# Kernel tuning notes

Hardware: AMD Instinct MI355X
Metric: run time of the kernel (lower is better)

## Reference

```python
import jax, jax.numpy as jnp
import numpy as np

N = 20000          # nodes
E = 320000         # edges (avg degree 16)
MUL = 64           # multiplicity of 0e and 1o in hidden irreps
NUM_BASIS = 8
HID = 64           # radial MLP hidden
NSPEC = 4          # node attribute (species) scalars
N_NEIGH = 16.0
SILU_NORM = 1.679177  # e3nn normalize2mom constant for silu


def silu_n(x):
    return jax.nn.silu(x) * SILU_NORM


def setup_inputs() -> dict:
    key = jax.random.key(0)
    ks = jax.random.split(key, 20)
    inp = {
        'node_scalars': jax.random.normal(ks[0], (N, MUL), jnp.float32),
        'node_vectors': jax.random.normal(ks[1], (N, MUL, 3), jnp.float32),
        'node_attr': jax.random.uniform(ks[2], (N, NSPEC), jnp.float32),
        'edge_sh': jax.random.normal(ks[3], (E, 4), jnp.float32),
        'edge_embedded': jax.random.uniform(ks[4], (E, NUM_BASIS), jnp.float32),
        'edge_src': jax.random.randint(ks[5], (E,), 0, N),
        'edge_dst': jax.random.randint(ks[6], (E,), 0, N),
        # e3nn Linear #1 (64x0e+64x1o -> same)
        'W_lin1_s': jax.random.normal(ks[7], (MUL, MUL), jnp.float32),
        'W_lin1_v': jax.random.normal(ks[8], (MUL, MUL), jnp.float32),
        # radial FullyConnectedNet 8 -> 64 -> 64 -> 256
        'W_fc0': jax.random.normal(ks[9], (NUM_BASIS, HID), jnp.float32),
        'W_fc1': jax.random.normal(ks[10], (HID, HID), jnp.float32),
        'W_fc2': jax.random.normal(ks[11], (HID, 4 * MUL), jnp.float32),
        # e3nn Linear #2 (128x0e+128x1o -> 128x0e+64x1o)
        'W_lin2_s': jax.random.normal(ks[12], (2 * MUL, 2 * MUL), jnp.float32),
        'W_lin2_v': jax.random.normal(ks[13], (2 * MUL, MUL), jnp.float32),
        # self-connection FullyConnectedTensorProduct weights
        'W_sc_s': jax.random.normal(ks[14], (MUL, NSPEC, 2 * MUL), jnp.float32),
        'W_sc_v': jax.random.normal(ks[15], (MUL, NSPEC, MUL), jnp.float32),
    }
    return inp


def reference(node_scalars, node_vectors, node_attr, edge_sh, edge_embedded,
              W_lin1_s, W_lin1_v, W_fc0, W_fc1, W_fc2, W_lin2_s, W_lin2_v,
              W_sc_s, W_sc_v, edge_src, edge_dst):
    inv_sqrt3 = 1.0 / jnp.sqrt(jnp.float32(3.0))
    # ---- self connection (FullyConnectedTensorProduct with scalar attrs) ----
    sc_norm = 1.0 / jnp.sqrt(jnp.float32(MUL * NSPEC))
    sc_s = jnp.einsum('nu,nv,uvw->nw', node_scalars, node_attr, W_sc_s) * sc_norm   # [N,128]
    sc_v = jnp.einsum('nui,nv,uvw->nwi', node_vectors, node_attr, W_sc_v) * sc_norm  # [N,64,3]
    # ---- e3nn Linear #1 ----
    lin_norm = 1.0 / jnp.sqrt(jnp.float32(MUL))
    s = (node_scalars @ W_lin1_s) * lin_norm                      # [N,64]
    v = jnp.einsum('nui,uw->nwi', node_vectors, W_lin1_v) * lin_norm  # [N,64,3]
    # ---- gather to edges ----
    s_e = s[edge_src]          # [E,64]
    v_e = v[edge_src]          # [E,64,3]
    y0 = edge_sh[:, :1]        # [E,1]  (0e)
    y1 = edge_sh[:, 1:4]       # [E,3]  (1o)
    # ---- radial MLP -> per-edge TP weights ----
    h = silu_n((edge_embedded @ W_fc0) / jnp.sqrt(jnp.float32(NUM_BASIS)))
    h = silu_n((h @ W_fc1) / jnp.sqrt(jnp.float32(HID)))
    w = (h @ W_fc2) / jnp.sqrt(jnp.float32(HID))                  # [E,256]
    wA, wB, wC, wD = w[:, :MUL], w[:, MUL:2*MUL], w[:, 2*MUL:3*MUL], w[:, 3*MUL:]
    # ---- per-edge CG tensor product ('uvu', component normalization) ----
    oA = wA * s_e * y0                                            # 0e x 0e -> 0e  [E,64]
    oD = wD * jnp.einsum('eui,ei->eu', v_e, y1) * inv_sqrt3       # 1o x 1o -> 0e  [E,64]
    oB = wB[:, :, None] * s_e[:, :, None] * y1[:, None, :]        # 0e x 1o -> 1o  [E,64,3]
    oC = wC[:, :, None] * v_e * y0[:, :, None]                    # 1o x 0e -> 1o  [E,64,3]
    # ---- scatter-sum to destination nodes, normalize by neighbors ----
    s_agg = jax.ops.segment_sum(jnp.concatenate([oA, oD], axis=-1), edge_dst, num_segments=N) / N_NEIGH  # [N,128]
    v_agg = jax.ops.segment_sum(jnp.concatenate([oB, oC], axis=1), edge_dst, num_segments=N) / N_NEIGH   # [N,128,3]
    # ---- e3nn Linear #2 (128x0e+128x1o -> 128x0e+64x1o) ----
    lin2_norm = 1.0 / jnp.sqrt(jnp.float32(2 * MUL))
    s_h = (s_agg @ W_lin2_s) * lin2_norm                          # [N,128]
    v_h = jnp.einsum('nui,uw->nwi', v_agg, W_lin2_v) * lin2_norm  # [N,64,3]
    # ---- self connection ----
    s_h = s_h + sc_s
    v_h = v_h + sc_v
    # ---- Gate (even irreps -> normalized silu) ----
    out_s = silu_n(s_h[:, :MUL])                                  # scalars [N,64]
    out_v = silu_n(s_h[:, MUL:])[:, :, None] * v_h                # gated vectors [N,64,3]
    return jnp.concatenate([out_s, out_v.reshape(out_v.shape[0], MUL * 3)], axis=-1)  # [N,256]
```

## Files before the change

### kernel.cpp

```cpp
#include <hip/hip_runtime.h>
#include <math.h>

#define N_NODES 20000
#define N_EDGES 320000
#define MUL 64
#define NUM_BASIS 8
#define HID 64
#define NSPEC 4

#define LIN_NORM     0.125f
#define INV_SQRT8    0.3535533906f
#define LIN2_NORM    0.08838834765f
#define SC_NORM      0.0625f
#define INV_NEIGH    0.0625f
#define INV_SQRT3    0.5773502692f
#define SILU_NORM    1.679177f

typedef __attribute__((ext_vector_type(8))) short bf16x8;
typedef __attribute__((ext_vector_type(4))) float f32x4;

__device__ __forceinline__ float silu_n(float x) {
    float s = 1.0f / (1.0f + __expf(-x));
    return x * s * SILU_NORM;
}

__device__ __forceinline__ float bcast(float x, int l) {
    return __uint_as_float(__builtin_amdgcn_readlane(__float_as_uint(x), l));
}
__device__ __forceinline__ int bcast_i(int x, int l) {
    return __builtin_amdgcn_readlane(x, l);
}

__device__ __forceinline__ unsigned short f2bf(float x) {
    unsigned int u = __float_as_uint(x);
    unsigned int r = (u + 0x7fffu + ((u >> 16) & 1u)) >> 16;
    return (unsigned short)r;
}

__device__ __forceinline__ unsigned int cvtpk(float lo, float hi) {
    unsigned int r;
    asm("v_cvt_pk_bf16_f32 %0, %1, %2" : "=v"(r) : "v"(lo), "v"(hi));
    return r;
}

__device__ __forceinline__ bf16x8 cvt8(float f0, float f1, float f2, float f3,
                                       float f4, float f5, float f6, float f7) {
    union { unsigned int u[4]; bf16x8 v; } r;
    r.u[0] = cvtpk(f0, f1);
    r.u[1] = cvtpk(f2, f3);
    r.u[2] = cvtpk(f4, f5);
    r.u[3] = cvtpk(f6, f7);
    return r.v;
}

#define WPREP_BLOCKS 51
__global__ __launch_bounds__(256) void k_pre(
    const float* __restrict__ W1, const float* __restrict__ W2,
    const float* __restrict__ Wl2s, const float* __restrict__ Wl2v,
    const float* __restrict__ Wscs, const float* __restrict__ Wscv,
    const float* __restrict__ W0,
    const float* __restrict__ Wl1s, const float* __restrict__ Wl1v,
    unsigned short* __restrict__ w1f, unsigned short* __restrict__ w2f,
    unsigned short* __restrict__ bsf, unsigned short* __restrict__ bvf,
    unsigned short* __restrict__ w0f,
    unsigned short* __restrict__ l1sf, unsigned short* __restrict__ l1vf,
    float4* __restrict__ agg4, int* __restrict__ counts)
{
    if (blockIdx.x >= WPREP_BLOCKS) {
        int idx = (blockIdx.x - WPREP_BLOCKS) * 256 + threadIdx.x;
        int nthr = (gridDim.x - WPREP_BLOCKS) * 256;
        const size_t total4 = (size_t)N_NODES * 128;
        float4 z = {0.f, 0.f, 0.f, 0.f};
        for (size_t i = idx; i < total4; i += nthr) agg4[i] = z;
        if (idx < N_NODES) counts[idx] = 0;
        return;
    }
    int t = blockIdx.x * 256 + threadIdx.x;
    if (t < 512) {
        int f = t >> 6, lane = t & 63;
        int kt = f >> 2, nt = f & 3, q = lane >> 4, c = lane & 15;
        #pragma unroll
        for (int j = 0; j < 8; ++j) {
            int k = kt * 32 + q * 8 + j;
            int n = nt * 16 + c;
            w1f[(size_t)t * 8 + j] = f2bf(W1[k * 64 + n]);
        }
    } else if (t < 2560) {
        int tt = t - 512;
        int f = tt >> 6, lane = tt & 63;
        int kt = f >> 4, nt = f & 15, q = lane >> 4, c = lane & 15;
        #pragma unroll
        for (int j = 0; j < 8; ++j) {
            int k = kt * 32 + q * 8 + j;
            int n = nt * 16 + c;
            w2f[(size_t)tt * 8 + j] = f2bf(W2[k * 256 + n]);
        }
    } else if (t < 4608) {
        int tt = t - 2560;
        int f = tt >> 6, lane = tt & 63;
        int kt = f >> 3, nt = f & 7, q = lane >> 4, c = lane & 15;
        #pragma unroll
        for (int j = 0; j < 8; ++j) {
            int k = kt * 32 + q * 8 + j;
            int n = nt * 16 + c;
            bsf[(size_t)tt * 8 + j] = f2bf(Wl2s[k * 128 + n] * LIN2_NORM);
        }
    } else if (t < 8704) {
        int tt = t - 4608;
        int f = tt >> 6, lane = tt & 63;
        int v = f >> 4, g = f & 15;
        int kt = g >> 3, nt = g & 7, q = lane >> 4, c = lane & 15;
        #pragma unroll
        for (int j = 0; j < 8; ++j) {
            int u = kt * 32 + q * 8 + j;
            int n = nt * 16 + c;
            bsf[(size_t)(2048 + tt) * 8 + j] = f2bf(Wscs[(u * 4 + v) * 128 + n] * SC_NORM);
        }
    } else if (t < 9728) {
        int tt = t - 8704;
        int f = tt >> 6, lane = tt & 63;
        int kt = f >> 2, nt = f & 3, q = lane >> 4, c = lane & 15;
        #pragma unroll
        for (int j = 0; j < 8; ++j) {
            int k = kt * 32 + q * 8 + j;
            int n = nt * 16 + c;
            bvf[(size_t)tt * 8 + j] = f2bf(Wl2v[k * 64 + n] * LIN2_NORM);
        }
    } else if (t < 11776) {
        int tt = t - 9728;
        int f = tt >> 6, lane = tt & 63;
        int v = f >> 3, g = f & 7;
        int kt = g >> 2, nt = g & 3, q = lane >> 4, c = lane & 15;
        #pragma unroll
        for (int j = 0; j < 8; ++j) {
            int u = kt * 32 + q * 8 + j;
            int n = nt * 16 + c;
            bvf[(size_t)(1024 + tt) * 8 + j] = f2bf(Wscv[(u * 4 + v) * 64 + n] * SC_NORM);
        }
    } else if (t < 12032) {
        int tt = t - 11776;
        int f = tt >> 6, lane = tt & 63;
        int q = lane >> 4, c = lane & 15;
        #pragma unroll
        for (int j = 0; j < 8; ++j) {
            int k = q * 8 + j;
            int n = f * 16 + c;
            w0f[(size_t)tt * 8 + j] =
                (k < 8) ? f2bf(W0[k * 64 + n] * INV_SQRT8) : (unsigned short)0;
        }
    } else if (t < 12544) {
        int tt = t - 12032;
        int f = tt >> 6, lane = tt & 63;
        int kt = f >> 2, nt = f & 3, q = lane >> 4, c = lane & 15;
        #pragma unroll
        for (int j = 0; j < 8; ++j) {
            int k = kt * 32 + q * 8 + j;
            int n = nt * 16 + c;
            l1sf[(size_t)tt * 8 + j] = f2bf(Wl1s[k * 64 + n] * LIN_NORM);
        }
    } else if (t < 13056) {
        int tt = t - 12544;
        int f = tt >> 6, lane = tt & 63;
        int kt = f >> 2, nt = f & 3, q = lane >> 4, c = lane & 15;
        #pragma unroll
        for (int j = 0; j < 8; ++j) {
            int k = kt * 32 + q * 8 + j;
            int n = nt * 16 + c;
            l1vf[(size_t)tt * 8 + j] = f2bf(Wl1v[k * 64 + n] * LIN_NORM);
        }
    }
}

__global__ __launch_bounds__(256) void k_hist(const int* __restrict__ edst,
                                              int* __restrict__ counts)
{
    int e = blockIdx.x * blockDim.x + threadIdx.x;
    if (e < N_EDGES) atomicAdd(&counts[edst[e]], 1);
}

#define SCAN_T 1024
__global__ __launch_bounds__(SCAN_T) void k_scan(const int* __restrict__ counts,
                                                 int* __restrict__ cursor)
{
    __shared__ int part[SCAN_T];
    int t = threadIdx.x;
    const int CH = (N_NODES + SCAN_T - 1) / SCAN_T;
    int b0 = t * CH;
    int s = 0;
    for (int i = 0; i < CH; ++i) {
        int idx = b0 + i;
        if (idx < N_NODES) s += counts[idx];
    }
    part[t] = s;
    __syncthreads();
    for (int off = 1; off < SCAN_T; off <<= 1) {
        int v = (t >= off) ? part[t - off] : 0;
        __syncthreads();
        part[t] += v;
        __syncthreads();
    }
    int run = (t == 0) ? 0 : part[t - 1];
    for (int i = 0; i < CH; ++i) {
        int idx = b0 + i;
        if (idx < N_NODES) {
            cursor[idx] = run;
            run += counts[idx];
        }
    }
}

#define FILL_BLOCKS 1250
__global__ __launch_bounds__(256) void k_fill_lin1(
    const int* __restrict__ edst, const int* __restrict__ esrc,
    const float* __restrict__ sh, const float* __restrict__ emb,
    int* __restrict__ cursor,
    int* __restrict__ dlist, int* __restrict__ slist,
    float4* __restrict__ ysort, float4* __restrict__ esort,
    const float* __restrict__ ns, const float* __restrict__ nv,
    const unsigned short* __restrict__ l1sf, const unsigned short* __restrict__ l1vf,
    float* __restrict__ s_out, float* __restrict__ v_out)
{
    if (blockIdx.x < FILL_BLOCKS) {
        int e = blockIdx.x * blockDim.x + threadIdx.x;
        if (e < N_EDGES) {
            int d = edst[e];
            int pos = atomicAdd(&cursor[d], 1);
            dlist[pos] = d;
            slist[pos] = esrc[e];
            ysort[pos] = ((const float4*)sh)[e];
            esort[(size_t)pos * 2]     = ((const float4*)emb)[(size_t)e * 2];
            esort[(size_t)pos * 2 + 1] = ((const float4*)emb)[(size_t)e * 2 + 1];
        }
        return;
    }
    const size_t NV = (size_t)N_NODES * 64;
    int lane = threadIdx.x & 63;
    int gwave = ((blockIdx.x - FILL_BLOCKS) * 256 + threadIdx.x) >> 6;
    int part = __builtin_amdgcn_readfirstlane(gwave & 3);
    int n0 = __builtin_amdgcn_readfirstlane((gwave >> 2) * 16);
    if (n0 >= N_NODES) return;
    int q = lane >> 4, c = lane & 15;
    int node = n0 + c;

    if (part == 0) {
        f32x4 Ds[4];
        #pragma unroll
        for (int nt = 0; nt < 4; ++nt) Ds[nt] = (f32x4){0.f, 0.f, 0.f, 0.f};
        #pragma unroll
        for (int kt = 0; kt < 2; ++kt) {
            const float* ap = ns + (size_t)node * 64 + kt * 32 + q * 8;
            float4 a0 = *(const float4*)ap;
            float4 a1 = *(const float4*)(ap + 4);
            bf16x8 A = cvt8(a0.x, a0.y, a0.z, a0.w, a1.x, a1.y, a1.z, a1.w);
            #pragma unroll
            for (int nt = 0; nt < 4; ++nt) {
                bf16x8 B = *(const bf16x8*)(l1sf + (size_t)((kt * 4 + nt) * 64 + lane) * 8);
                Ds[nt] = __builtin_amdgcn_mfma_f32_16x16x32_bf16(A, B, Ds[nt], 0, 0, 0);
            }
        }
        #pragma unroll
        for (int nt = 0; nt < 4; ++nt)
            #pragma unroll
            for (int r = 0; r < 4; ++r)
                s_out[(size_t)(n0 + q * 4 + r) * 64 + nt * 16 + c] = Ds[nt][r];
    } else {
        int p = part - 1;
        f32x4 Dv[4];
        #pragma unroll
        for (int nt = 0; nt < 4; ++nt) Dv[nt] = (f32x4){0.f, 0.f, 0.f, 0.f};
        #pragma unroll
        for (int kt = 0; kt < 2; ++kt) {
            float f[8];
            #pragma unroll
            for (int j = 0; j < 8; ++j)
                f[j] = nv[(size_t)node * 192 + (size_t)(kt * 32 + q * 8 + j) * 3 + p];
            bf16x8 A = cvt8(f[0], f[1], f[2], f[3], f[4], f[5], f[6], f[7]);
            #pragma unroll
            for (int nt = 0; nt < 4; ++nt) {
                bf16x8 B = *(const bf16x8*)(l1vf + (size_t)((kt * 4 + nt) * 64 + lane) * 8);
                Dv[nt] = __builtin_amdgcn_mfma_f32_16x16x32_bf16(A, B, Dv[nt], 0, 0, 0);
            }
        }
        #pragma unroll
        for (int nt = 0; nt < 4; ++nt)
            #pragma unroll
            for (int r = 0; r < 4; ++r)
                v_out[p * NV + (size_t)(n0 + q * 4 + r) * 64 + nt * 16 + c] = Dv[nt][r];
    }
}

__global__ __launch_bounds__(256) void k_edge_fused(
    const float* __restrict__ esort,
    const unsigned short* __restrict__ w0f,
    const unsigned short* __restrict__ w1f, const unsigned short* __restrict__ w2f,
    const int* __restrict__ slist, const int* __restrict__ dlist,
    const float* __restrict__ ysort,
    const float* __restrict__ s_in, const float* __restrict__ v_in,
    float* __restrict__ s_agg, float* __restrict__ v_agg)
{
    const size_t NP2 = (size_t)N_NODES * 128;
    const size_t NV  = (size_t)N_NODES * 64;

    __shared__ __align__(16) unsigned char pool[4 * 8832];

    int lane = threadIdx.x & 63;
    int wid  = threadIdx.x >> 6;
    int q = lane >> 4;
    int c = lane & 15;
    int lbase = __builtin_amdgcn_readfirstlane(blockIdx.x * 256 + wid * 64);
    unsigned char* base = pool + wid * 8832;
    unsigned short* myh0 = (unsigned short*)base;
    unsigned short* myh1 = (unsigned short*)(base + 2304);
    unsigned int*   myw1 = (unsigned int*)base;
    unsigned int*   myw2 = (unsigned int*)(base + 4608);

    int srcv = slist[lbase + lane];
    int dstv = dlist[lbase + lane];
    float4 y4 = ((const float4*)ysort)[lbase + lane];

    bf16x8 B0[4];
    #pragma unroll
    for (int f = 0; f < 4; ++f)
        B0[f] = *(const bf16x8*)(w0f + (size_t)(f * 64 + lane) * 8);
    bf16x8 B1[2][4];
    #pragma unroll
    for (int f = 0; f < 8; ++f)
        B1[f >> 2][f & 3] = *(const bf16x8*)(w1f + (size_t)(f * 64 + lane) * 8);

    const float4* e4 = (const float4*)esort;
    const float WS  = 0.125f * INV_NEIGH;
    const float WSD = WS * INV_SQRT3;

    float accA = 0.f, aB0 = 0.f, aB1 = 0.f, aB2 = 0.f;
    float accD = 0.f, aC0 = 0.f, aC1 = 0.f, aC2 = 0.f;
    int cur = bcast_i(dstv, 0);

    #pragma unroll 1
    for (int mt = 0; mt < 4; ++mt) {
        int tb16 = mt * 16;

        float4 ea = {0.f, 0.f, 0.f, 0.f}, eb = {0.f, 0.f, 0.f, 0.f};
        if (q == 0) {
            ea = e4[(size_t)(lbase + tb16 + c) * 2];
            eb = e4[(size_t)(lbase + tb16 + c) * 2 + 1];
        }
        bf16x8 Ae = cvt8(ea.x, ea.y, ea.z, ea.w, eb.x, eb.y, eb.z, eb.w);
        f32x4 D0[4];
        #pragma unroll
        for (int nt = 0; nt < 4; ++nt) {
            f32x4 z = {0.f, 0.f, 0.f, 0.f};
            D0[nt] = __builtin_amdgcn_mfma_f32_16x16x32_bf16(Ae, B0[nt], z, 0, 0, 0);
        }
        #pragma unroll
        for (int nt = 0; nt < 4; ++nt)
            #pragma unroll
            for (int r = 0; r < 4; ++r)
                myh0[(q * 4 + r) * 72 + nt * 16 + c] = f2bf(silu_n(D0[nt][r]));
        __builtin_amdgcn_s_waitcnt(0xC07F);
        bf16x8 A0[2];
        #pragma unroll
        for (int kt = 0; kt < 2; ++kt)
            A0[kt] = *(const bf16x8*)(myh0 + c * 72 + kt * 32 + q * 8);

        f32x4 D1[4];
        #pragma unroll
        for (int nt = 0; nt < 4; ++nt) {
            f32x4 z = {0.f, 0.f, 0.f, 0.f};
            D1[nt] = __builtin_amdgcn_mfma_f32_16x16x32_bf16(A0[0], B1[0][nt], z, 0, 0, 0);
            D1[nt] = __builtin_amdgcn_mfma_f32_16x16x32_bf16(A0[1], B1[1][nt], D1[nt], 0, 0, 0);
        }
        #pragma unroll
        for (int nt = 0; nt < 4; ++nt)
            #pragma unroll
            for (int r = 0; r < 4; ++r)
                myh1[(q * 4 + r) * 72 + nt * 16 + c] = f2bf(silu_n(D1[nt][r] * 0.125f));
        __builtin_amdgcn_s_waitcnt(0xC07F);
        bf16x8 A1[2];
        #pragma unroll
        for (int kt = 0; kt < 2; ++kt)
            A1[kt] = *(const bf16x8*)(myh1 + c * 72 + kt * 32 + q * 8);

        #pragma unroll
        for (int half = 0; half < 2; ++half) {
            int ga = half * 2, gb = half * 2 + 1;
            f32x4 Da[4], Db[4];
            #pragma unroll
            for (int ntl = 0; ntl < 4; ++ntl) {
                bf16x8 b0 = *(const bf16x8*)(w2f + (size_t)((ga * 4 + ntl) * 64 + lane) * 8);
                bf16x8 b1 = *(const bf16x8*)(w2f + (size_t)((16 + ga * 4 + ntl) * 64 + lane) * 8);
                f32x4 z = {0.f, 0.f, 0.f, 0.f};
                Da[ntl] = __builtin_amdgcn_mfma_f32_16x16x32_bf16(A1[0], b0, z, 0, 0, 0);
                Da[ntl] = __builtin_amdgcn_mfma_f32_16x16x32_bf16(A1[1], b1, Da[ntl], 0, 0, 0);
            }
            #pragma unroll
            for (int ntl = 0; ntl < 4; ++ntl) {
                bf16x8 b0 = *(const bf16x8*)(w2f + (size_t)((gb * 4 + ntl) * 64 + lane) * 8);
                bf16x8 b1 = *(const bf16x8*)(w2f + (size_t)((16 + gb * 4 + ntl) * 64 + lane) * 8);
                f32x4 z = {0.f, 0.f, 0.f, 0.f};
                Db[ntl] = __builtin_amdgcn_mfma_f32_16x16x32_bf16(A1[0], b0, z, 0, 0, 0);
                Db[ntl] = __builtin_amdgcn_mfma_f32_16x16x32_bf16(A1[1], b1, Db[ntl], 0, 0, 0);
            }
            float sb = half ? WSD : WS;
            unsigned int* pp = half ? myw2 : myw1;
            #pragma unroll
            for (int ntl = 0; ntl < 4; ++ntl)
                #pragma unroll
                for (int r = 0; r < 4; ++r)
                    pp[(q * 4 + r) * 66 + ntl * 16 + c] = cvtpk(Da[ntl][r] * WS, Db[ntl][r] * sb);
        }
        __builtin_amdgcn_s_waitcnt(0xC07F);

        #pragma unroll 1
        for (int ebl = 0; ebl < 16; ebl += 8) {
            float se8[8], v08[8], v18[8], v28[8];
            unsigned int wab[8], wcd[8];
            #pragma unroll
            for (int i = 0; i < 8; ++i) {
                int et = ebl + i;
                int src = bcast_i(srcv, tb16 + et);
                wab[i] = myw1[et * 66 + lane];
                wcd[i] = myw2[et * 66 + lane];
                se8[i] = s_in[(size_t)src * 64 + lane];
                v08[i] = v_in[0 * NV + (size_t)src * 64 + lane];
                v18[i] = v_in[1 * NV + (size_t)src * 64 + lane];
                v28[i] = v_in[2 * NV + (size_t)src * 64 + lane];
            }
            #pragma unroll
            for (int i = 0; i < 8; ++i) {
                int e = tb16 + ebl + i;
                int dst = bcast_i(dstv, e);
                float y0 = bcast(y4.x, e), yx = bcast(y4.y, e);
                float yy = bcast(y4.z, e), yz = bcast(y4.w, e);
                if (dst != cur) {
                    size_t db = (size_t)cur * 128;
                    unsafeAtomicAdd(&s_agg[db + lane], accA);
                    unsafeAtomicAdd(&s_agg[db + 64 + lane], accD);
                    unsafeAtomicAdd(&v_agg[0 * NP2 + db + lane], aB0);
                    unsafeAtomicAdd(&v_agg[1 * NP2 + db + lane], aB1);
                    unsafeAtomicAdd(&v_agg[2 * NP2 + db + lane], aB2);
                    unsafeAtomicAdd(&v_agg[0 * NP2 + db + 64 + lane], aC0);
                    unsafeAtomicAdd(&v_agg[1 * NP2 + db + 64 + lane], aC1);
                    unsafeAtomicAdd(&v_agg[2 * NP2 + db + 64 + lane], aC2);
                    accA = aB0 = aB1 = aB2 = 0.f;
                    accD = aC0 = aC1 = aC2 = 0.f;
                    cur = dst;
                }
                float wA = __uint_as_float(wab[i] << 16);
                float wB = __uint_as_float(wab[i] & 0xffff0000u);
                float wC = __uint_as_float(wcd[i] << 16);
                float wD = __uint_as_float(wcd[i] & 0xffff0000u);
                accA = fmaf(wA, se8[i] * y0, accA);
                float bB = wB * se8[i];
                aB0 = fmaf(bB, yx, aB0);
                aB1 = fmaf(bB, yy, aB1);
                aB2 = fmaf(bB, yz, aB2);
                float dot = v08[i] * yx + v18[i] * yy + v28[i] * yz;
                accD = fmaf(wD, dot, accD);
                float bC = wC * y0;
                aC0 = fmaf(bC, v08[i], aC0);
                aC1 = fmaf(bC, v18[i], aC1);
                aC2 = fmaf(bC, v28[i], aC2);
            }
        }
    }
    {
        size_t db = (size_t)cur * 128;
        unsafeAtomicAdd(&s_agg[db + lane], accA);
        unsafeAtomicAdd(&s_agg[db + 64 + lane], accD);
        unsafeAtomicAdd(&v_agg[0 * NP2 + db + lane], aB0);
        unsafeAtomicAdd(&v_agg[1 * NP2 + db + lane], aB1);
        unsafeAtomicAdd(&v_agg[2 * NP2 + db + lane], aB2);
        unsafeAtomicAdd(&v_agg[0 * NP2 + db + 64 + lane], aC0);
        unsafeAtomicAdd(&v_agg[1 * NP2 + db + 64 + lane], aC1);
        unsafeAtomicAdd(&v_agg[2 * NP2 + db + 64 + lane], aC2);
    }
}

__global__ __launch_bounds__(256) void k_node_out_s(
    const float* __restrict__ ns, const float* __restrict__ na,
    const unsigned short* __restrict__ bsf,
    const float* __restrict__ s_agg,
    float* __restrict__ out, float* __restrict__ gbuf)
{
    int lane = threadIdx.x & 63;
    int wtile = (blockIdx.x * blockDim.x + threadIdx.x) >> 6;
    int n0 = __builtin_amdgcn_readfirstlane(wtile * 16);
    if (n0 >= N_NODES) return;
    int q = lane >> 4, c = lane & 15;
    int node = n0 + c;

    float pa[4];
    #pragma unroll
    for (int v = 0; v < 4; ++v) pa[v] = na[(size_t)node * 4 + v];

    f32x4 Ds[8];
    #pragma unroll
    for (int nt = 0; nt < 8; ++nt) Ds[nt] = (f32x4){0.f, 0.f, 0.f, 0.f};

    #pragma unroll
    for (int kt = 0; kt < 4; ++kt) {
        const float* ap = s_agg + (size_t)node * 128 + kt * 32 + q * 8;
        float4 a0 = *(const float4*)ap;
        float4 a1 = *(const float4*)(ap + 4);
        bf16x8 A;
        A[0] = (short)f2bf(a0.x); A[1] = (short)f2bf(a0.y);
        A[2] = (short)f2bf(a0.z); A[3] = (short)f2bf(a0.w);
        A[4] = (short)f2bf(a1.x); A[5] = (short)f2bf(a1.y);
        A[6] = (short)f2bf(a1.z); A[7] = (short)f2bf(a1.w);
        #pragma unroll
        for (int nt = 0; nt < 8; ++nt) {
            bf16x8 B = *(const bf16x8*)(bsf + (size_t)((kt * 8 + nt) * 64 + lane) * 8);
            Ds[nt] = __builtin_amdgcn_mfma_f32_16x16x32_bf16(A, B, Ds[nt], 0, 0, 0);
        }
    }
    {
        const float* np_ = ns + (size_t)node * 64 + q * 8;
        float4 n00 = *(const float4*)np_;
        float4 n01 = *(const float4*)(np_ + 4);
        float4 n10 = *(const float4*)(np_ + 32);
        float4 n11 = *(const float4*)(np_ + 36);
        float nsr[16] = {n00.x, n00.y, n00.z, n00.w, n01.x, n01.y, n01.z, n01.w,
                         n10.x, n10.y, n10.z, n10.w, n11.x, n11.y, n11.z, n11.w};
        #pragma unroll
        for (int v = 0; v < 4; ++v) {
            float sv = pa[v];
            #pragma unroll
            for (int kt = 0; kt < 2; ++kt) {
                bf16x8 A;
                #pragma unroll
                for (int j = 0; j < 8; ++j)
                    A[j] = (short)f2bf(nsr[kt * 8 + j] * sv);
                #pragma unroll
                for (int nt = 0; nt < 8; ++nt) {
                    bf16x8 B = *(const bf16x8*)(bsf +
                        (size_t)((32 + v * 16 + kt * 8 + nt) * 64 + lane) * 8);
                    Ds[nt] = __builtin_amdgcn_mfma_f32_16x16x32_bf16(A, B, Ds[nt], 0, 0, 0);
                }
            }
        }
    }
    #pragma unroll
    for (int nt = 0; nt < 4; ++nt)
        #pragma unroll
        for (int r = 0; r < 4; ++r) {
            out[(size_t)(n0 + q * 4 + r) * 256 + nt * 16 + c] = silu_n(Ds[nt][r]);
            gbuf[(size_t)(n0 + q * 4 + r) * 64 + nt * 16 + c] = silu_n(Ds[4 + nt][r]);
        }
}

__global__ __launch_bounds__(256) void k_node_out_v(
    const float* __restrict__ nv, const float* __restrict__ na,
    const unsigned short* __restrict__ bvf,
    const float* __restrict__ v_agg, const float* __restrict__ gbuf,
    float* __restrict__ out)
{
    const size_t NP2 = (size_t)N_NODES * 128;
    int lane = threadIdx.x & 63;
    int gwave = (blockIdx.x * blockDim.x + threadIdx.x) >> 6;
    if (gwave >= 3750) return;
    int p = __builtin_amdgcn_readfirstlane(gwave % 3);
    int n0 = __builtin_amdgcn_readfirstlane((gwave / 3) * 16);
    int q = lane >> 4, c = lane & 15;
    int node = n0 + c;

    float pa[4];
    #pragma unroll
    for (int v = 0; v < 4; ++v) pa[v] = na[(size_t)node * 4 + v];

    f32x4 Dv[4];
    #pragma unroll
    for (int nt = 0; nt < 4; ++nt) Dv[nt] = (f32x4){0.f, 0.f, 0.f, 0.f};

    #pragma unroll
    for (int kt = 0; kt < 4; ++kt) {
        const float* ap = v_agg + (size_t)p * NP2 + (size_t)node * 128 + kt * 32 + q * 8;
        float4 a0 = *(const float4*)ap;
        float4 a1 = *(const float4*)(ap + 4);
        bf16x8 A;
        A[0] = (short)f2bf(a0.x); A[1] = (short)f2bf(a0.y);
        A[2] = (short)f2bf(a0.z); A[3] = (short)f2bf(a0.w);
        A[4] = (short)f2bf(a1.x); A[5] = (short)f2bf(a1.y);
        A[6] = (short)f2bf(a1.z); A[7] = (short)f2bf(a1.w);
        #pragma unroll
        for (int nt = 0; nt < 4; ++nt) {
            bf16x8 B = *(const bf16x8*)(bvf + (size_t)((kt * 4 + nt) * 64 + lane) * 8);
            Dv[nt] = __builtin_amdgcn_mfma_f32_16x16x32_bf16(A, B, Dv[nt], 0, 0, 0);
        }
    }
    float nvr[16];
    #pragma unroll
    for (int j = 0; j < 8; ++j) {
        nvr[j]     = nv[(size_t)node * 192 + (size_t)(q * 8 + j) * 3 + p];
        nvr[8 + j] = nv[(size_t)node * 192 + (size_t)(32 + q * 8 + j) * 3 + p];
    }
    #pragma unroll
    for (int v = 0; v < 4; ++v) {
        float sv = pa[v];
        #pragma unroll
        for (int kt = 0; kt < 2; ++kt) {
            bf16x8 A;
            #pragma unroll
            for (int j = 0; j < 8; ++j)
                A[j] = (short)f2bf(nvr[kt * 8 + j] * sv);
            #pragma unroll
            for (int nt = 0; nt < 4; ++nt) {
                bf16x8 B = *(const bf16x8*)(bvf +
                    (size_t)((16 + v * 8 + kt * 4 + nt) * 64 + lane) * 8);
                Dv[nt] = __builtin_amdgcn_mfma_f32_16x16x32_bf16(A, B, Dv[nt], 0, 0, 0);
            }
        }
    }
    #pragma unroll
    for (int nt = 0; nt < 4; ++nt)
        #pragma unroll
        for (int r = 0; r < 4; ++r) {
            int w = nt * 16 + c;
            float g = gbuf[(size_t)(n0 + q * 4 + r) * 64 + w];
            out[(size_t)(n0 + q * 4 + r) * 256 + 64 + (size_t)w * 3 + p] = g * Dv[nt][r];
        }
}

extern "C" void kernel_launch(void* const* d_in, const int* in_sizes, int n_in,
                              void* d_out, int out_size, void* d_ws, size_t ws_size,
                              hipStream_t stream)
{
    const float* node_scalars = (const float*)d_in[0];
    const float* node_vectors = (const float*)d_in[1];
    const float* node_attr    = (const float*)d_in[2];
    const float* edge_sh      = (const float*)d_in[3];
    const float* edge_emb     = (const float*)d_in[4];
    const int*   edge_src     = (const int*)d_in[5];
    const int*   edge_dst     = (const int*)d_in[6];
    const float* W_lin1_s = (const float*)d_in[7];
    const float* W_lin1_v = (const float*)d_in[8];
    const float* W_fc0    = (const float*)d_in[9];
    const float* W_fc1    = (const float*)d_in[10];
    const float* W_fc2    = (const float*)d_in[11];
    const float* W_lin2_s = (const float*)d_in[12];
    const float* W_lin2_v = (const float*)d_in[13];
    const float* W_sc_s   = (const float*)d_in[14];
    const float* W_sc_v   = (const float*)d_in[15];
    float* out = (float*)d_out;

    float* ws    = (float*)d_ws;
    float* s_agg = ws;
    float* v_agg = s_agg + (size_t)N_NODES * 128;
    float* s_buf = v_agg + 3 * (size_t)N_NODES * 128;
    float* v_buf = s_buf + (size_t)N_NODES * 64;
    float* gbuf  = v_buf + 3 * (size_t)N_NODES * 64;
    int*   counts = (int*)(gbuf + (size_t)N_NODES * 64);
    int*   cursor = counts + N_NODES;
    int*   dlist  = cursor + N_NODES;
    int*   slist  = dlist + N_EDGES;
    unsigned short* w1f  = (unsigned short*)(slist + N_EDGES);
    unsigned short* w2f  = w1f + 4096;
    unsigned short* bsf  = w2f + 16384;
    unsigned short* bvf  = bsf + 49152;
    unsigned short* w0f  = bvf + 24576;
    unsigned short* l1sf = w0f + 2048;
    unsigned short* l1vf = l1sf + 4096;
    float4* ysort = (float4*)(l1vf + 4096);
    float4* esort = ysort + N_EDGES;

    {
        k_pre<<<WPREP_BLOCKS + 2048, 256, 0, stream>>>(
            W_fc1, W_fc2, W_lin2_s, W_lin2_v, W_sc_s, W_sc_v,
            W_fc0, W_lin1_s, W_lin1_v,
            w1f, w2f, bsf, bvf, w0f, l1sf, l1vf,
            (float4*)s_agg, counts);
    }
    {
        int blocks = (N_EDGES + 255) / 256;
        k_hist<<<blocks, 256, 0, stream>>>(edge_dst, counts);
    }
    k_scan<<<1, SCAN_T, 0, stream>>>(counts, cursor);
    {
        k_fill_lin1<<<FILL_BLOCKS + 1250, 256, 0, stream>>>(
            edge_dst, edge_src, edge_sh, edge_emb, cursor,
            dlist, slist, ysort, esort,
            node_scalars, node_vectors, l1sf, l1vf, s_buf, v_buf);
    }
    {
        int blocks = N_EDGES / 256;
        k_edge_fused<<<blocks, 256, 0, stream>>>((const float*)esort, w0f, w1f, w2f,
                                                 slist, dlist, (const float*)ysort,
                                                 s_buf, v_buf, s_agg, v_agg);
    }
    {
        int blocks = (1250 + 3) / 4;
        k_node_out_s<<<blocks, 256, 0, stream>>>(node_scalars, node_attr, bsf,
                                                 s_agg, out, gbuf);
    }
    {
        int blocks = (3750 + 3) / 4;
        k_node_out_v<<<blocks, 256, 0, stream>>>(node_vectors, node_attr, bvf,
                                                 v_agg, gbuf, out);
    }
}
```

Before: 318.4 us.

## Pack lin1 node features into interleaved bf16x4 for edge gathers

The lin1 outputs (scalar plus three vector components) are now stored as bf16 and interleaved per (node, channel) into one 8-byte ushort4. Previously they lived in four separate fp32 arrays. The edge kernel now gathers each source node's features with a single 8-byte load per lane instead of four 4-byte loads from separate arrays. This cuts gather bandwidth and the number of memory transactions in the scatter-heavy edge loop. In exchange, intermediate precision drops to bf16, and the fill kernel writes scattered 2-byte stores.

```diff
diff --git a/kernel.cpp b/kernel.cpp
--- a/kernel.cpp
+++ b/kernel.cpp
@@ -35,6 +35,10 @@
     unsigned int u = __float_as_uint(x);
     unsigned int r = (u + 0x7fffu + ((u >> 16) & 1u)) >> 16;
     return (unsigned short)r;
+}
+
+__device__ __forceinline__ float bf2f(unsigned short u) {
+    return __uint_as_float((unsigned int)u << 16);
 }
 
 __device__ __forceinline__ unsigned int cvtpk(float lo, float hi) {
@@ -218,7 +222,7 @@
     float4* __restrict__ ysort, float4* __restrict__ esort,
     const float* __restrict__ ns, const float* __restrict__ nv,
     const unsigned short* __restrict__ l1sf, const unsigned short* __restrict__ l1vf,
-    float* __restrict__ s_out, float* __restrict__ v_out)
+    unsigned short* __restrict__ svp)
 {
     if (blockIdx.x < FILL_BLOCKS) {
         int e = blockIdx.x * blockDim.x + threadIdx.x;
@@ -233,7 +237,6 @@
         }
         return;
     }
-    const size_t NV = (size_t)N_NODES * 64;
     int lane = threadIdx.x & 63;
     int gwave = ((blockIdx.x - FILL_BLOCKS) * 256 + threadIdx.x) >> 6;
     int part = __builtin_amdgcn_readfirstlane(gwave & 3);
@@ -262,7 +265,7 @@
         for (int nt = 0; nt < 4; ++nt)
             #pragma unroll
             for (int r = 0; r < 4; ++r)
-                s_out[(size_t)(n0 + q * 4 + r) * 64 + nt * 16 + c] = Ds[nt][r];
+                svp[((size_t)(n0 + q * 4 + r) * 64 + nt * 16 + c) * 4 + 0] = f2bf(Ds[nt][r]);
     } else {
         int p = part - 1;
         f32x4 Dv[4];
@@ -285,7 +288,7 @@
         for (int nt = 0; nt < 4; ++nt)
             #pragma unroll
             for (int r = 0; r < 4; ++r)
-                v_out[p * NV + (size_t)(n0 + q * 4 + r) * 64 + nt * 16 + c] = Dv[nt][r];
+                svp[((size_t)(n0 + q * 4 + r) * 64 + nt * 16 + c) * 4 + 1 + p] = f2bf(Dv[nt][r]);
     }
 }
 
@@ -295,11 +298,10 @@
     const unsigned short* __restrict__ w1f, const unsigned short* __restrict__ w2f,
     const int* __restrict__ slist, const int* __restrict__ dlist,
     const float* __restrict__ ysort,
-    const float* __restrict__ s_in, const float* __restrict__ v_in,
+    const ushort4* __restrict__ svp,
     float* __restrict__ s_agg, float* __restrict__ v_agg)
 {
     const size_t NP2 = (size_t)N_NODES * 128;
-    const size_t NV  = (size_t)N_NODES * 64;
 
     __shared__ __align__(16) unsigned char pool[4 * 8832];
 
@@ -412,7 +414,7 @@
 
         #pragma unroll 1
         for (int ebl = 0; ebl < 16; ebl += 8) {
-            float se8[8], v08[8], v18[8], v28[8];
+            ushort4 sv8[8];
             unsigned int wab[8], wcd[8];
             #pragma unroll
             for (int i = 0; i < 8; ++i) {
@@ -420,10 +422,7 @@
                 int src = bcast_i(srcv, tb16 + et);
                 wab[i] = myw1[et * 66 + lane];
                 wcd[i] = myw2[et * 66 + lane];
-                se8[i] = s_in[(size_t)src * 64 + lane];
-                v08[i] = v_in[0 * NV + (size_t)src * 64 + lane];
-                v18[i] = v_in[1 * NV + (size_t)src * 64 + lane];
-                v28[i] = v_in[2 * NV + (size_t)src * 64 + lane];
+                sv8[i] = svp[(size_t)src * 64 + lane];
             }
             #pragma unroll
             for (int i = 0; i < 8; ++i) {
@@ -445,21 +444,25 @@
                     accD = aC0 = aC1 = aC2 = 0.f;
                     cur = dst;
                 }
+                float se = bf2f(sv8[i].x);
+                float v0 = bf2f(sv8[i].y);
+                float v1 = bf2f(sv8[i].z);
+                float v2 = bf2f(sv8[i].w);
                 float wA = __uint_as_float(wab[i] << 16);
                 float wB = __uint_as_float(wab[i] & 0xffff0000u);
                 float wC = __uint_as_float(wcd[i] << 16);
                 float wD = __uint_as_float(wcd[i] & 0xffff0000u);
-                accA = fmaf(wA, se8[i] * y0, accA);
-                float bB = wB * se8[i];
+                accA = fmaf(wA, se * y0, accA);
+                float bB = wB * se;
                 aB0 = fmaf(bB, yx, aB0);
                 aB1 = fmaf(bB, yy, aB1);
                 aB2 = fmaf(bB, yz, aB2);
-                float dot = v08[i] * yx + v18[i] * yy + v28[i] * yz;
+                float dot = v0 * yx + v1 * yy + v2 * yz;
                 accD = fmaf(wD, dot, accD);
                 float bC = wC * y0;
-                aC0 = fmaf(bC, v08[i], aC0);
-                aC1 = fmaf(bC, v18[i], aC1);
-                aC2 = fmaf(bC, v28[i], aC2);
+                aC0 = fmaf(bC, v0, aC0);
+                aC1 = fmaf(bC, v1, aC1);
+                aC2 = fmaf(bC, v2, aC2);
             }
         }
     }
@@ -645,9 +648,8 @@
     float* ws    = (float*)d_ws;
     float* s_agg = ws;
     float* v_agg = s_agg + (size_t)N_NODES * 128;
-    float* s_buf = v_agg + 3 * (size_t)N_NODES * 128;
-    float* v_buf = s_buf + (size_t)N_NODES * 64;
-    float* gbuf  = v_buf + 3 * (size_t)N_NODES * 64;
+    unsigned short* svp = (unsigned short*)(v_agg + 3 * (size_t)N_NODES * 128);
+    float* gbuf  = (float*)(svp + (size_t)N_NODES * 256);
     int*   counts = (int*)(gbuf + (size_t)N_NODES * 64);
     int*   cursor = counts + N_NODES;
     int*   dlist  = cursor + N_NODES;
@@ -678,13 +680,13 @@
         k_fill_lin1<<<FILL_BLOCKS + 1250, 256, 0, stream>>>(
             edge_dst, edge_src, edge_sh, edge_emb, cursor,
             dlist, slist, ysort, esort,
-            node_scalars, node_vectors, l1sf, l1vf, s_buf, v_buf);
+            node_scalars, node_vectors, l1sf, l1vf, svp);
     }
     {
         int blocks = N_EDGES / 256;
         k_edge_fused<<<blocks, 256, 0, stream>>>((const float*)esort, w0f, w1f, w2f,
                                                  slist, dlist, (const float*)ysort,
-                                                 s_buf, v_buf, s_agg, v_agg);
+                                                 (const ushort4*)svp, s_agg, v_agg);
     }
     {
         int blocks = (1250 + 3) / 4;
```

After: 306.3 us. 1.04x faster.
